# Performance work log

Hardware: AMD Instinct MI355X
Metric: run time of the kernel (lower is better)

The kernel has to match this reference:

```python
import jax, jax.numpy as jnp
import numpy as np

N_NODES = 100000
N_EDGES = 1600000
IN_FEATS = 256
OUT_FEATS = 128


def setup_inputs() -> dict:
    key = jax.random.key(0)
    k1, k2, k3, k4, k5 = jax.random.split(key, 5)
    x = jax.random.normal(k1, (N_NODES, IN_FEATS), dtype=jnp.float32)
    edge_row = jax.random.randint(k2, (N_EDGES,), 0, N_NODES, dtype=jnp.int64 if jax.config.jax_enable_x64 else jnp.int32)
    edge_col = jax.random.randint(k3, (N_EDGES,), 0, N_NODES, dtype=jnp.int64 if jax.config.jax_enable_x64 else jnp.int32)
    edge_val = jax.random.uniform(k4, (N_EDGES,), dtype=jnp.float32)
    # xavier_uniform-like init for weight
    limit = float(np.sqrt(6.0 / (IN_FEATS + OUT_FEATS)))
    weight = jax.random.uniform(k5, (IN_FEATS, OUT_FEATS), dtype=jnp.float32, minval=-limit, maxval=limit)
    b = jnp.zeros((OUT_FEATS,), dtype=jnp.float32)
    return {"x": x, "edge_row": edge_row, "edge_col": edge_col, "edge_val": edge_val, "weight": weight, "b": b}


def reference(x, edge_row, edge_col, edge_val, weight, b):
    # sup = input @ weight : [N, out_feats]
    sup = x @ weight
    # out = spmm(adj, sup): gather source rows, scale by edge value, scatter-add to dest
    msgs = edge_val[:, None] * sup[edge_col]          # [E, out_feats]
    out = jax.ops.segment_sum(msgs, edge_row, num_segments=N_NODES)  # [N, out_feats]
    return out + b
```

## Files before the change

kernel.cpp:

```cpp
#include <hip/hip_runtime.h>


#define K_FEATS 256
#define N_FEATS 128
#define BSHIFT 7
#define BROWS 128
#define BCAP 3072
#define STASH 12
#define CHUNK 8192
#define EPT 32
#define RMOD 5

typedef __attribute__((ext_vector_type(8))) short short8;
typedef __attribute__((ext_vector_type(4))) float float4v;

__device__ __forceinline__ unsigned short f2bf(float f) {
    unsigned int u = __float_as_uint(f);
    unsigned int r = u + 0x7FFF + ((u >> 16) & 1);
    return (unsigned short)(r >> 16);
}

__global__ __launch_bounds__(256) void prep_w(const float* __restrict__ w,
                                              unsigned short* __restrict__ wt) {
    int n = blockIdx.x;
    int k = threadIdx.x;
    wt[n * K_FEATS + k] = f2bf(w[k * N_FEATS + n]);
}

__global__ __launch_bounds__(256) void zero_ints(int* __restrict__ p, int n) {
    int i = blockIdx.x * 256 + threadIdx.x;
    if (i < n) p[i] = 0;
}

__global__ __launch_bounds__(256) void gemm_partition(
        const float* __restrict__ x, const unsigned short* __restrict__ wt,
        unsigned short* __restrict__ sup, int M, int NT,
        const int* __restrict__ erow, const int* __restrict__ ecol,
        const float* __restrict__ eval_, int* __restrict__ bcur,
        int2* __restrict__ tmp, int E, int NB, int NCH) {
    __shared__ int hist[1024];
    __shared__ int cur[1024];
    const int g   = blockIdx.x;
    const int tid = threadIdx.x;

    if (g % RMOD == 0) {
        int pid = g / RMOD;
        if (pid >= NCH) return;
        const long e0 = (long)pid * CHUNK;

        for (int i = tid; i < NB; i += 256) hist[i] = 0;
        __syncthreads();

        int rows[EPT];
#pragma unroll
        for (int i = 0; i < EPT; i++) {
            long e = e0 + tid + i * 256;
            int r = -1;
            if (e < E) {
                r = erow[e];
                atomicAdd(&hist[r >> BSHIFT], 1);
            }
            rows[i] = r;
        }
        __syncthreads();

        for (int i = tid; i < NB; i += 256) {
            int c = hist[i];
            cur[i] = c ? atomicAdd(&bcur[i], c) : 0;
        }
        __syncthreads();

#pragma unroll
        for (int i = 0; i < EPT; i++) {
            long e = e0 + tid + i * 256;
            if (e >= E) continue;
            int r = rows[i];
            int b = r >> BSHIFT;
            int p = atomicAdd(&cur[b], 1);
            if (p < BCAP)
                tmp[(long)b * BCAP + p] = make_int2(((r & (BROWS - 1)) << 17) | ecol[e],
                                                    __float_as_int(eval_[e]));
        }
        return;
    }

    int tile = g - g / RMOD - 1;
    if (tile >= NT) return;

    const int wv   = tid >> 6;
    const int lane = tid & 63;
    const int l15  = lane & 15;
    const int quad = lane >> 4;
    const int row0 = tile * 128 + wv * 32;

    float4v acc[2][8];
#pragma unroll
    for (int mt = 0; mt < 2; mt++)
#pragma unroll
        for (int nt = 0; nt < 8; nt++) acc[mt][nt] = (float4v)(0.f);

#pragma unroll 2
    for (int k0 = 0; k0 < K_FEATS; k0 += 32) {
        short8 afrag[2];
#pragma unroll
        for (int mt = 0; mt < 2; mt++) {
            int grow = row0 + mt * 16 + l15;
            float4 a0 = make_float4(0.f, 0.f, 0.f, 0.f);
            float4 a1 = make_float4(0.f, 0.f, 0.f, 0.f);
            if (grow < M) {
                const float* p = x + (long)grow * K_FEATS + k0 + quad * 8;
                a0 = *(const float4*)p;
                a1 = *(const float4*)(p + 4);
            }
            short8 af;
            af[0] = (short)f2bf(a0.x); af[1] = (short)f2bf(a0.y);
            af[2] = (short)f2bf(a0.z); af[3] = (short)f2bf(a0.w);
            af[4] = (short)f2bf(a1.x); af[5] = (short)f2bf(a1.y);
            af[6] = (short)f2bf(a1.z); af[7] = (short)f2bf(a1.w);
            afrag[mt] = af;
        }
        short8 bfrag[8];
#pragma unroll
        for (int nt = 0; nt < 8; nt++) {
            bfrag[nt] = *(const short8*)(wt + (nt * 16 + l15) * K_FEATS + k0 + quad * 8);
        }
#pragma unroll
        for (int mt = 0; mt < 2; mt++)
#pragma unroll
            for (int nt = 0; nt < 8; nt++)
                acc[mt][nt] = __builtin_amdgcn_mfma_f32_16x16x32_bf16(
                    afrag[mt], bfrag[nt], acc[mt][nt], 0, 0, 0);
    }

#pragma unroll
    for (int mt = 0; mt < 2; mt++) {
#pragma unroll
        for (int reg = 0; reg < 4; reg++) {
            int grow = row0 + mt * 16 + quad * 4 + reg;
            if (grow < M) {
#pragma unroll
                for (int nt = 0; nt < 8; nt++) {
                    sup[(long)grow * N_FEATS + nt * 16 + l15] = f2bf(acc[mt][nt][reg]);
                }
            }
        }
    }
}

__global__ __launch_bounds__(256) void bucket_spmm(const int* __restrict__ bcnt,
                                                   const int2* __restrict__ tmp,
                                                   const unsigned short* __restrict__ sup,
                                                   const float* __restrict__ b,
                                                   float* __restrict__ out, int M) {
    __shared__ int hist[BROWS];
    __shared__ int rs[BROWS];
    __shared__ int cur[BROWS];
    __shared__ __align__(16) int2 se[BCAP];
    const int bkt  = blockIdx.x;
    const int tid  = threadIdx.x;
    const int wv   = tid >> 6;
    const int lane = tid & 63;
    const int row0 = bkt << BSHIFT;

    if (tid < BROWS) hist[tid] = 0;
    __syncthreads();

    int cnt = bcnt[bkt];
    if (cnt > BCAP) cnt = BCAP;
    const int2* t = tmp + (long)bkt * BCAP;

    int2 stash[STASH];
#pragma unroll
    for (int j = 0; j < STASH; j++) {
        int i = tid + j * 256;
        if (i < cnt) {
            int2 e = t[i];
            stash[j] = e;
            atomicAdd(&hist[(unsigned)e.x >> 17], 1);
        }
    }
    __syncthreads();

    if (tid < BROWS) cur[tid] = hist[tid];
    __syncthreads();
#pragma unroll
    for (int s = 1; s < BROWS; s <<= 1) {
        int v = 0;
        if (tid >= s && tid < BROWS) v = cur[tid - s];
        __syncthreads();
        if (tid < BROWS) cur[tid] += v;
        __syncthreads();
    }
    if (tid < BROWS) {
        int start = cur[tid] - hist[tid];
        rs[tid]  = start;
        cur[tid] = start;
    }
    __syncthreads();

#pragma unroll
    for (int j = 0; j < STASH; j++) {
        int i = tid + j * 256;
        if (i < cnt) {
            int2 e = stash[j];
            int rl = (unsigned)e.x >> 17;
            int p = atomicAdd(&cur[rl], 1);
            se[p] = make_int2(e.x & 0x1FFFF, e.y);
        }
    }
    __syncthreads();

    const int half = lane >> 5;
    const int l31  = lane & 31;
    const uint2* sup64 = (const uint2*)sup;
    const float4v bb = ((const float4v*)b)[l31];

    for (int rr = 0; rr < 32; rr++) {
        int r    = wv * 32 + rr;
        int grow = row0 + r;
        if (grow >= M) break;
        int s  = rs[r];
        int e2 = s + hist[r];

        float4v acc = (float4v)(0.f);
        int base = s;
        for (; base + 8 <= e2; base += 8) {
            int2 ed[4];
#pragma unroll
            for (int u = 0; u < 4; u++) ed[u] = se[base + half + 2 * u];
            uint2 g[4];
#pragma unroll
            for (int u = 0; u < 4; u++) g[u] = sup64[(long)ed[u].x * 32 + l31];
#pragma unroll
            for (int u = 0; u < 4; u++) {
                float v = __int_as_float(ed[u].y);
                acc.x += v * __uint_as_float(g[u].x << 16);
                acc.y += v * __uint_as_float(g[u].x & 0xFFFF0000u);
                acc.z += v * __uint_as_float(g[u].y << 16);
                acc.w += v * __uint_as_float(g[u].y & 0xFFFF0000u);
            }
        }
        for (int i = base + half; i < e2; i += 2) {
            int2 ed = se[i];
            uint2 g = sup64[(long)ed.x * 32 + l31];
            float v = __int_as_float(ed.y);
            acc.x += v * __uint_as_float(g.x << 16);
            acc.y += v * __uint_as_float(g.x & 0xFFFF0000u);
            acc.z += v * __uint_as_float(g.y << 16);
            acc.w += v * __uint_as_float(g.y & 0xFFFF0000u);
        }

        acc.x += __shfl_xor(acc.x, 32);
        acc.y += __shfl_xor(acc.y, 32);
        acc.z += __shfl_xor(acc.z, 32);
        acc.w += __shfl_xor(acc.w, 32);

        if (half == 0) {
            float4v o = acc + bb;
            *(float4v*)(out + (long)grow * N_FEATS + l31 * 4) = o;
        }
    }
}

extern "C" void kernel_launch(void* const* d_in, const int* in_sizes, int n_in,
                              void* d_out, int out_size, void* d_ws, size_t ws_size,
                              hipStream_t stream) {
    const float* x     = (const float*)d_in[0];
    const int*   erow  = (const int*)d_in[1];
    const int*   ecol  = (const int*)d_in[2];
    const float* eval_ = (const float*)d_in[3];
    const float* w     = (const float*)d_in[4];
    const float* b     = (const float*)d_in[5];
    float* out = (float*)d_out;

    const int M   = in_sizes[0] / K_FEATS;
    const int E   = in_sizes[1];
    const int NB  = (M + BROWS - 1) >> BSHIFT;
    const int NT  = (M + 127) / 128;
    const int NCH = (E + CHUNK - 1) / CHUNK;

    size_t o_sup  = 0;
    size_t o_wt   = o_sup  + (((size_t)M * N_FEATS * 2 + 15) & ~15ul);
    size_t o_bcur = o_wt   + (size_t)K_FEATS * N_FEATS * 2;
    size_t o_tmp  = o_bcur + (((size_t)NB * 4 + 15) & ~15ul);

    unsigned short* sup  = (unsigned short*)((char*)d_ws + o_sup);
    unsigned short* wt   = (unsigned short*)((char*)d_ws + o_wt);
    int*            bcur = (int*)((char*)d_ws + o_bcur);
    int2*           tmp  = (int2*)((char*)d_ws + o_tmp);

    prep_w<<<N_FEATS, 256, 0, stream>>>(w, wt);
    zero_ints<<<(NB + 255) / 256, 256, 0, stream>>>(bcur, NB);

    gemm_partition<<<NT + NCH, 256, 0, stream>>>(x, wt, sup, M, NT,
                                                 erow, ecol, eval_, bcur, tmp, E, NB, NCH);

    bucket_spmm<<<NB, 256, 0, stream>>>(bcur, tmp, sup, b, out, M);
}
```

Measured before the change: 317.5 us.

## Shrink SpMM buckets to 64 rows and software-pipeline GEMM A-fragment loads

Halves the bucket size used by the edge partition and bucketed SpMM (64 rows per bucket, smaller capacity and stash, larger shared histogram) so there are twice as many smaller blocks, raising parallelism and lowering per-block LDS use. Separately, the GEMM inner loop is fully unrolled and prefetches the next K-slice of x into registers while converting and issuing MFMAs on the current slice, to hide global load latency. The costs are more register pressure and more buckets to histogram, plus a greater chance of overflowing the reduced bucket capacity on skewed row distributions. The final prefetch wraps to k=0 and performs a redundant load.

```diff
diff --git a/kernel.cpp b/kernel.cpp
--- a/kernel.cpp
+++ b/kernel.cpp
@@ -3,10 +3,11 @@
 
 #define K_FEATS 256
 #define N_FEATS 128
-#define BSHIFT 7
-#define BROWS 128
-#define BCAP 3072
-#define STASH 12
+#define BSHIFT 6
+#define BROWS 64
+#define BCAP 1792
+#define STASH 7
+#define NBPAD 2048
 #define CHUNK 8192
 #define EPT 32
 #define RMOD 5
@@ -38,8 +39,8 @@
         const int* __restrict__ erow, const int* __restrict__ ecol,
         const float* __restrict__ eval_, int* __restrict__ bcur,
         int2* __restrict__ tmp, int E, int NB, int NCH) {
-    __shared__ int hist[1024];
-    __shared__ int cur[1024];
+    __shared__ int hist[NBPAD];
+    __shared__ int cur[NBPAD];
     const int g   = blockIdx.x;
     const int tid = threadIdx.x;
 
@@ -92,6 +93,12 @@
     const int l15  = lane & 15;
     const int quad = lane >> 4;
     const int row0 = tile * 128 + wv * 32;
+    const int grow0 = row0 + l15;
+    const int grow1 = row0 + 16 + l15;
+    const bool ok0 = grow0 < M;
+    const bool ok1 = grow1 < M;
+    const float* p0 = x + (long)grow0 * K_FEATS + quad * 8;
+    const float* p1 = x + (long)grow1 * K_FEATS + quad * 8;
 
     float4v acc[2][8];
 #pragma unroll
@@ -99,30 +106,35 @@
 #pragma unroll
         for (int nt = 0; nt < 8; nt++) acc[mt][nt] = (float4v)(0.f);
 
-#pragma unroll 2
+    float4 ca[2][2];
+    ca[0][0] = ok0 ? *(const float4*)p0 : make_float4(0.f, 0.f, 0.f, 0.f);
+    ca[0][1] = ok0 ? *(const float4*)(p0 + 4) : make_float4(0.f, 0.f, 0.f, 0.f);
+    ca[1][0] = ok1 ? *(const float4*)p1 : make_float4(0.f, 0.f, 0.f, 0.f);
+    ca[1][1] = ok1 ? *(const float4*)(p1 + 4) : make_float4(0.f, 0.f, 0.f, 0.f);
+
+#pragma unroll
     for (int k0 = 0; k0 < K_FEATS; k0 += 32) {
-        short8 afrag[2];
-#pragma unroll
-        for (int mt = 0; mt < 2; mt++) {
-            int grow = row0 + mt * 16 + l15;
-            float4 a0 = make_float4(0.f, 0.f, 0.f, 0.f);
-            float4 a1 = make_float4(0.f, 0.f, 0.f, 0.f);
-            if (grow < M) {
-                const float* p = x + (long)grow * K_FEATS + k0 + quad * 8;
-                a0 = *(const float4*)p;
-                a1 = *(const float4*)(p + 4);
-            }
-            short8 af;
-            af[0] = (short)f2bf(a0.x); af[1] = (short)f2bf(a0.y);
-            af[2] = (short)f2bf(a0.z); af[3] = (short)f2bf(a0.w);
-            af[4] = (short)f2bf(a1.x); af[5] = (short)f2bf(a1.y);
-            af[6] = (short)f2bf(a1.z); af[7] = (short)f2bf(a1.w);
-            afrag[mt] = af;
-        }
+        const int kn = (k0 + 32) & (K_FEATS - 1);
+        float4 na[2][2];
+        na[0][0] = ok0 ? *(const float4*)(p0 + kn) : make_float4(0.f, 0.f, 0.f, 0.f);
+        na[0][1] = ok0 ? *(const float4*)(p0 + kn + 4) : make_float4(0.f, 0.f, 0.f, 0.f);
+        na[1][0] = ok1 ? *(const float4*)(p1 + kn) : make_float4(0.f, 0.f, 0.f, 0.f);
+        na[1][1] = ok1 ? *(const float4*)(p1 + kn + 4) : make_float4(0.f, 0.f, 0.f, 0.f);
+
         short8 bfrag[8];
 #pragma unroll
         for (int nt = 0; nt < 8; nt++) {
             bfrag[nt] = *(const short8*)(wt + (nt * 16 + l15) * K_FEATS + k0 + quad * 8);
+        }
+        short8 afrag[2];
+#pragma unroll
+        for (int mt = 0; mt < 2; mt++) {
+            short8 af;
+            af[0] = (short)f2bf(ca[mt][0].x); af[1] = (short)f2bf(ca[mt][0].y);
+            af[2] = (short)f2bf(ca[mt][0].z); af[3] = (short)f2bf(ca[mt][0].w);
+            af[4] = (short)f2bf(ca[mt][1].x); af[5] = (short)f2bf(ca[mt][1].y);
+            af[6] = (short)f2bf(ca[mt][1].z); af[7] = (short)f2bf(ca[mt][1].w);
+            afrag[mt] = af;
         }
 #pragma unroll
         for (int mt = 0; mt < 2; mt++)
@@ -130,6 +142,11 @@
             for (int nt = 0; nt < 8; nt++)
                 acc[mt][nt] = __builtin_amdgcn_mfma_f32_16x16x32_bf16(
                     afrag[mt], bfrag[nt], acc[mt][nt], 0, 0, 0);
+#pragma unroll
+        for (int mt = 0; mt < 2; mt++) {
+            ca[mt][0] = na[mt][0];
+            ca[mt][1] = na[mt][1];
+        }
     }
 
 #pragma unroll
@@ -215,8 +232,8 @@
     const uint2* sup64 = (const uint2*)sup;
     const float4v bb = ((const float4v*)b)[l31];
 
-    for (int rr = 0; rr < 32; rr++) {
-        int r    = wv * 32 + rr;
+    for (int rr = 0; rr < 16; rr++) {
+        int r    = wv * 16 + rr;
         int grow = row0 + r;
         if (grow >= M) break;
         int s  = rs[r];
```

After: 312.8 us. About the same (-1.5%).

## Stage GEMM weights in swizzled LDS and double SpMM block size

Applied to the files above, without the earlier changes.

The GEMM tiles now cooperatively load the bf16 weight matrix into shared memory in two K-halves, using an XOR swizzle to avoid bank conflicts. B fragments are then read from LDS instead of every wave re-reading them from global memory. The bucket SpMM kernel moves to 512 threads per block with half the stash per thread and 16 rows per wave, which raises parallelism per bucket. The cost is a 32KB shared allocation in the fused kernel, which may cut occupancy, plus extra barriers.

```diff
diff --git a/kernel.cpp b/kernel.cpp
--- a/kernel.cpp
+++ b/kernel.cpp
@@ -6,7 +6,7 @@
 #define BSHIFT 7
 #define BROWS 128
 #define BCAP 3072
-#define STASH 12
+#define STASH 6
 #define CHUNK 8192
 #define EPT 32
 #define RMOD 5
@@ -38,14 +38,15 @@
         const int* __restrict__ erow, const int* __restrict__ ecol,
         const float* __restrict__ eval_, int* __restrict__ bcur,
         int2* __restrict__ tmp, int E, int NB, int NCH) {
-    __shared__ int hist[1024];
-    __shared__ int cur[1024];
+    __shared__ __align__(16) unsigned char smem[32768];
     const int g   = blockIdx.x;
     const int tid = threadIdx.x;
 
     if (g % RMOD == 0) {
         int pid = g / RMOD;
         if (pid >= NCH) return;
+        int* hist = (int*)smem;
+        int* cur  = (int*)(smem + 4096);
         const long e0 = (long)pid * CHUNK;
 
         for (int i = tid; i < NB; i += 256) hist[i] = 0;
@@ -87,11 +88,18 @@
     int tile = g - g / RMOD - 1;
     if (tile >= NT) return;
 
+    unsigned char* Bs = smem;
     const int wv   = tid >> 6;
     const int lane = tid & 63;
     const int l15  = lane & 15;
     const int quad = lane >> 4;
     const int row0 = tile * 128 + wv * 32;
+    const int grow0 = row0 + l15;
+    const int grow1 = row0 + 16 + l15;
+    const bool ok0 = grow0 < M;
+    const bool ok1 = grow1 < M;
+    const float* p0 = x + (long)grow0 * K_FEATS + quad * 8;
+    const float* p1 = x + (long)grow1 * K_FEATS + quad * 8;
 
     float4v acc[2][8];
 #pragma unroll
@@ -99,37 +107,56 @@
 #pragma unroll
         for (int nt = 0; nt < 8; nt++) acc[mt][nt] = (float4v)(0.f);
 
-#pragma unroll 2
-    for (int k0 = 0; k0 < K_FEATS; k0 += 32) {
-        short8 afrag[2];
-#pragma unroll
-        for (int mt = 0; mt < 2; mt++) {
-            int grow = row0 + mt * 16 + l15;
-            float4 a0 = make_float4(0.f, 0.f, 0.f, 0.f);
-            float4 a1 = make_float4(0.f, 0.f, 0.f, 0.f);
-            if (grow < M) {
-                const float* p = x + (long)grow * K_FEATS + k0 + quad * 8;
-                a0 = *(const float4*)p;
-                a1 = *(const float4*)(p + 4);
-            }
-            short8 af;
-            af[0] = (short)f2bf(a0.x); af[1] = (short)f2bf(a0.y);
-            af[2] = (short)f2bf(a0.z); af[3] = (short)f2bf(a0.w);
-            af[4] = (short)f2bf(a1.x); af[5] = (short)f2bf(a1.y);
-            af[6] = (short)f2bf(a1.z); af[7] = (short)f2bf(a1.w);
-            afrag[mt] = af;
-        }
-        short8 bfrag[8];
-#pragma unroll
-        for (int nt = 0; nt < 8; nt++) {
-            bfrag[nt] = *(const short8*)(wt + (nt * 16 + l15) * K_FEATS + k0 + quad * 8);
-        }
-#pragma unroll
-        for (int mt = 0; mt < 2; mt++)
-#pragma unroll
-            for (int nt = 0; nt < 8; nt++)
-                acc[mt][nt] = __builtin_amdgcn_mfma_f32_16x16x32_bf16(
-                    afrag[mt], bfrag[nt], acc[mt][nt], 0, 0, 0);
+    for (int ks = 0; ks < 2; ks++) {
+#pragma unroll
+        for (int it = 0; it < 8; it++) {
+            int idx = it * 256 + tid;
+            int n   = idx >> 4;
+            int c   = (idx & 15) << 4;
+            uint4 v = *(const uint4*)((const char*)wt + (long)n * 512 + ks * 256 + c);
+            int byte = (n << 8) + c;
+            *(uint4*)(Bs + (byte ^ ((n & 7) << 4))) = v;
+        }
+        __syncthreads();
+
+#pragma unroll
+        for (int kk = 0; kk < 128; kk += 32) {
+            const int k0 = ks * 128 + kk;
+            float4 a00 = ok0 ? *(const float4*)(p0 + k0) : make_float4(0.f, 0.f, 0.f, 0.f);
+            float4 a01 = ok0 ? *(const float4*)(p0 + k0 + 4) : make_float4(0.f, 0.f, 0.f, 0.f);
+            float4 a10 = ok1 ? *(const float4*)(p1 + k0) : make_float4(0.f, 0.f, 0.f, 0.f);
+            float4 a11 = ok1 ? *(const float4*)(p1 + k0 + 4) : make_float4(0.f, 0.f, 0.f, 0.f);
+
+            short8 bfrag[8];
+#pragma unroll
+            for (int nt = 0; nt < 8; nt++) {
+                int n    = nt * 16 + l15;
+                int byte = (n << 8) + (kk << 1) + (quad << 4);
+                bfrag[nt] = *(const short8*)(Bs + (byte ^ ((n & 7) << 4)));
+            }
+
+            short8 afrag[2];
+            {
+                short8 af;
+                af[0] = (short)f2bf(a00.x); af[1] = (short)f2bf(a00.y);
+                af[2] = (short)f2bf(a00.z); af[3] = (short)f2bf(a00.w);
+                af[4] = (short)f2bf(a01.x); af[5] = (short)f2bf(a01.y);
+                af[6] = (short)f2bf(a01.z); af[7] = (short)f2bf(a01.w);
+                afrag[0] = af;
+                af[0] = (short)f2bf(a10.x); af[1] = (short)f2bf(a10.y);
+                af[2] = (short)f2bf(a10.z); af[3] = (short)f2bf(a10.w);
+                af[4] = (short)f2bf(a11.x); af[5] = (short)f2bf(a11.y);
+                af[6] = (short)f2bf(a11.z); af[7] = (short)f2bf(a11.w);
+                afrag[1] = af;
+            }
+#pragma unroll
+            for (int mt = 0; mt < 2; mt++)
+#pragma unroll
+                for (int nt = 0; nt < 8; nt++)
+                    acc[mt][nt] = __builtin_amdgcn_mfma_f32_16x16x32_bf16(
+                        afrag[mt], bfrag[nt], acc[mt][nt], 0, 0, 0);
+        }
+        __syncthreads();
     }
 
 #pragma unroll
@@ -147,7 +174,7 @@
     }
 }
 
-__global__ __launch_bounds__(256) void bucket_spmm(const int* __restrict__ bcnt,
+__global__ __launch_bounds__(512) void bucket_spmm(const int* __restrict__ bcnt,
                                                    const int2* __restrict__ tmp,
                                                    const unsigned short* __restrict__ sup,
                                                    const float* __restrict__ b,
@@ -172,7 +199,7 @@
     int2 stash[STASH];
 #pragma unroll
     for (int j = 0; j < STASH; j++) {
-        int i = tid + j * 256;
+        int i = tid + j * 512;
         if (i < cnt) {
             int2 e = t[i];
             stash[j] = e;
@@ -200,7 +227,7 @@
 
 #pragma unroll
     for (int j = 0; j < STASH; j++) {
-        int i = tid + j * 256;
+        int i = tid + j * 512;
         if (i < cnt) {
             int2 e = stash[j];
             int rl = (unsigned)e.x >> 17;
@@ -215,8 +242,8 @@
     const uint2* sup64 = (const uint2*)sup;
     const float4v bb = ((const float4v*)b)[l31];
 
-    for (int rr = 0; rr < 32; rr++) {
-        int r    = wv * 32 + rr;
+    for (int rr = 0; rr < 16; rr++) {
+        int r    = wv * 16 + rr;
         int grow = row0 + r;
         if (grow >= M) break;
         int s  = rs[r];
@@ -295,5 +322,5 @@
     gemm_partition<<<NT + NCH, 256, 0, stream>>>(x, wt, sup, M, NT,
                                                  erow, ecol, eval_, bcur, tmp, E, NB, NCH);
 
-    bucket_spmm<<<NB, 256, 0, stream>>>(bcur, tmp, sup, b, out, M);
-}
+    bucket_spmm<<<NB, 512, 0, stream>>>(bcur, tmp, sup, b, out, M);
+}
```

Measured after the change: 304.1 us. 4.2% less time.

## Shrink GEMM tiles to 64 rows with prefetched A and widen spmm blocks to 512

Applied to the files above, without the earlier changes.

The fused GEMM/partition kernel now gives each wave one 16-row MFMA tile instead of two, so a block covers 64 rows and twice as many GEMM blocks are launched. The interleave ratio with partition blocks is adjusted to match. A rows are prefetched four k-steps ahead in registers to hide global load latency, at the cost of reloading the weight fragments twice as often per output row. The bucket spmm kernel moves from 256 to 512 threads per block with half the stash per thread and 16 rows per wave, to raise parallelism per bucket.

```diff
diff --git a/kernel.cpp b/kernel.cpp
--- a/kernel.cpp
+++ b/kernel.cpp
@@ -6,10 +6,10 @@
 #define BSHIFT 7
 #define BROWS 128
 #define BCAP 3072
-#define STASH 12
+#define STASH 6
 #define CHUNK 8192
 #define EPT 32
-#define RMOD 5
+#define RMOD 9
 
 typedef __attribute__((ext_vector_type(8))) short short8;
 typedef __attribute__((ext_vector_type(4))) float float4v;
@@ -91,33 +91,34 @@
     const int lane = tid & 63;
     const int l15  = lane & 15;
     const int quad = lane >> 4;
-    const int row0 = tile * 128 + wv * 32;
-
-    float4v acc[2][8];
-#pragma unroll
-    for (int mt = 0; mt < 2; mt++)
-#pragma unroll
-        for (int nt = 0; nt < 8; nt++) acc[mt][nt] = (float4v)(0.f);
-
-#pragma unroll 2
-    for (int k0 = 0; k0 < K_FEATS; k0 += 32) {
-        short8 afrag[2];
-#pragma unroll
-        for (int mt = 0; mt < 2; mt++) {
-            int grow = row0 + mt * 16 + l15;
-            float4 a0 = make_float4(0.f, 0.f, 0.f, 0.f);
-            float4 a1 = make_float4(0.f, 0.f, 0.f, 0.f);
-            if (grow < M) {
-                const float* p = x + (long)grow * K_FEATS + k0 + quad * 8;
-                a0 = *(const float4*)p;
-                a1 = *(const float4*)(p + 4);
-            }
-            short8 af;
-            af[0] = (short)f2bf(a0.x); af[1] = (short)f2bf(a0.y);
-            af[2] = (short)f2bf(a0.z); af[3] = (short)f2bf(a0.w);
-            af[4] = (short)f2bf(a1.x); af[5] = (short)f2bf(a1.y);
-            af[6] = (short)f2bf(a1.z); af[7] = (short)f2bf(a1.w);
-            afrag[mt] = af;
+    const int row0 = tile * 64 + wv * 16;
+    const int grow = row0 + l15;
+    const bool ok  = grow < M;
+    const float* pA = x + (long)grow * K_FEATS + quad * 8;
+    const float4 z4 = make_float4(0.f, 0.f, 0.f, 0.f);
+
+    float4v acc[8];
+#pragma unroll
+    for (int nt = 0; nt < 8; nt++) acc[nt] = (float4v)(0.f);
+
+    float4 ca[4][2];
+#pragma unroll
+    for (int s = 0; s < 4; s++) {
+        ca[s][0] = ok ? *(const float4*)(pA + s * 32)     : z4;
+        ca[s][1] = ok ? *(const float4*)(pA + s * 32 + 4) : z4;
+    }
+
+#pragma unroll
+    for (int s = 0; s < 8; s++) {
+        const int k0 = s * 32;
+        short8 af;
+        af[0] = (short)f2bf(ca[s & 3][0].x); af[1] = (short)f2bf(ca[s & 3][0].y);
+        af[2] = (short)f2bf(ca[s & 3][0].z); af[3] = (short)f2bf(ca[s & 3][0].w);
+        af[4] = (short)f2bf(ca[s & 3][1].x); af[5] = (short)f2bf(ca[s & 3][1].y);
+        af[6] = (short)f2bf(ca[s & 3][1].z); af[7] = (short)f2bf(ca[s & 3][1].w);
+        if (s < 4) {
+            ca[s & 3][0] = ok ? *(const float4*)(pA + (s + 4) * 32)     : z4;
+            ca[s & 3][1] = ok ? *(const float4*)(pA + (s + 4) * 32 + 4) : z4;
         }
         short8 bfrag[8];
 #pragma unroll
@@ -125,29 +126,23 @@
             bfrag[nt] = *(const short8*)(wt + (nt * 16 + l15) * K_FEATS + k0 + quad * 8);
         }
 #pragma unroll
-        for (int mt = 0; mt < 2; mt++)
-#pragma unroll
-            for (int nt = 0; nt < 8; nt++)
-                acc[mt][nt] = __builtin_amdgcn_mfma_f32_16x16x32_bf16(
-                    afrag[mt], bfrag[nt], acc[mt][nt], 0, 0, 0);
-    }
-
-#pragma unroll
-    for (int mt = 0; mt < 2; mt++) {
-#pragma unroll
-        for (int reg = 0; reg < 4; reg++) {
-            int grow = row0 + mt * 16 + quad * 4 + reg;
-            if (grow < M) {
-#pragma unroll
-                for (int nt = 0; nt < 8; nt++) {
-                    sup[(long)grow * N_FEATS + nt * 16 + l15] = f2bf(acc[mt][nt][reg]);
-                }
+        for (int nt = 0; nt < 8; nt++)
+            acc[nt] = __builtin_amdgcn_mfma_f32_16x16x32_bf16(af, bfrag[nt], acc[nt], 0, 0, 0);
+    }
+
+#pragma unroll
+    for (int reg = 0; reg < 4; reg++) {
+        int gr = row0 + quad * 4 + reg;
+        if (gr < M) {
+#pragma unroll
+            for (int nt = 0; nt < 8; nt++) {
+                sup[(long)gr * N_FEATS + nt * 16 + l15] = f2bf(acc[nt][reg]);
             }
         }
     }
 }
 
-__global__ __launch_bounds__(256) void bucket_spmm(const int* __restrict__ bcnt,
+__global__ __launch_bounds__(512) void bucket_spmm(const int* __restrict__ bcnt,
                                                    const int2* __restrict__ tmp,
                                                    const unsigned short* __restrict__ sup,
                                                    const float* __restrict__ b,
@@ -172,7 +167,7 @@
     int2 stash[STASH];
 #pragma unroll
     for (int j = 0; j < STASH; j++) {
-        int i = tid + j * 256;
+        int i = tid + j * 512;
         if (i < cnt) {
             int2 e = t[i];
             stash[j] = e;
@@ -200,7 +195,7 @@
 
 #pragma unroll
     for (int j = 0; j < STASH; j++) {
-        int i = tid + j * 256;
+        int i = tid + j * 512;
         if (i < cnt) {
             int2 e = stash[j];
             int rl = (unsigned)e.x >> 17;
@@ -215,8 +210,8 @@
     const uint2* sup64 = (const uint2*)sup;
     const float4v bb = ((const float4v*)b)[l31];
 
-    for (int rr = 0; rr < 32; rr++) {
-        int r    = wv * 32 + rr;
+    for (int rr = 0; rr < 16; rr++) {
+        int r    = wv * 16 + rr;
         int grow = row0 + r;
         if (grow >= M) break;
         int s  = rs[r];
@@ -276,7 +271,7 @@
     const int M   = in_sizes[0] / K_FEATS;
     const int E   = in_sizes[1];
     const int NB  = (M + BROWS - 1) >> BSHIFT;
-    const int NT  = (M + 127) / 128;
+    const int NT  = (M + 63) / 64;
     const int NCH = (E + CHUNK - 1) / CHUNK;
 
     size_t o_sup  = 0;
@@ -295,5 +290,5 @@
     gemm_partition<<<NT + NCH, 256, 0, stream>>>(x, wt, sup, M, NT,
                                                  erow, ecol, eval_, bcur, tmp, E, NB, NCH);
 
-    bucket_spmm<<<NB, 256, 0, stream>>>(bcur, tmp, sup, b, out, M);
-}
+    bucket_spmm<<<NB, 512, 0, stream>>>(bcur, tmp, sup, b, out, M);
+}
```

New measurement: 346.4 us. +9.1%, slower.
